# Kernel optimization log

Measured on AMD Instinct MI355X. Metric: run time of the kernel, lower is better.

The kernel has to match this reference:

```python
import jax, jax.numpy as jnp
import numpy as np

N = 50000      # num nodes
HID = 64       # hidden_dim
N2V = 64       # node2vec dim
E = 800000     # num edges
EP = 100000    # prediction edges
L = 2          # num_layers
EPS = 1e-5     # BatchNorm eps


def setup_inputs() -> dict:
    key = jax.random.key(0)
    ks = jax.random.split(key, 8)
    edge_index = jax.random.randint(ks[0], (2, E), 0, N)
    pred_edge = jax.random.randint(ks[1], (EP, 2), 0, N)
    id_emb = jax.random.normal(ks[2], (N, HID), jnp.float32) * 0.1      # learnable ID embedding
    n2v_emb = jax.random.normal(ks[3], (N, N2V), jnp.float32) * 0.1     # frozen node2vec embedding
    proj_w = jax.random.normal(ks[4], (HID + N2V, HID), jnp.float32) / np.sqrt(HID + N2V)
    proj_b = jnp.zeros((HID,), jnp.float32)
    conv_w = jax.random.normal(ks[5], (L, HID, HID), jnp.float32) / np.sqrt(HID)
    conv_b = jnp.zeros((L, HID), jnp.float32)
    bn_gamma = jnp.ones((L, HID), jnp.float32)
    bn_beta = jnp.zeros((L, HID), jnp.float32)
    return {"edge_index": edge_index, "pred_edge": pred_edge, "id_emb": id_emb,
            "n2v_emb": n2v_emb, "proj_w": proj_w, "proj_b": proj_b,
            "conv_w": conv_w, "conv_b": conv_b, "bn_gamma": bn_gamma, "bn_beta": bn_beta}


def reference(edge_index, pred_edge, id_emb, n2v_emb, proj_w, proj_b, conv_w, conv_b, bn_gamma, bn_beta):
    # input projection of concatenated embeddings: [N, HID+N2V] @ [HID+N2V, HID]
    x = jnp.concatenate([id_emb, n2v_emb], axis=1) @ proj_w + proj_b

    # GCN normalization with self-loops: norm_e = d^-1/2[src] * d^-1/2[dst]
    loops = jnp.arange(N, dtype=edge_index.dtype)
    row = jnp.concatenate([edge_index[0], loops])   # source nodes
    col = jnp.concatenate([edge_index[1], loops])   # destination nodes
    deg = jax.ops.segment_sum(jnp.ones(row.shape, x.dtype), col, num_segments=N)
    dis = jnp.where(deg > 0, jax.lax.rsqrt(deg), 0.0)
    norm = dis[row] * dis[col]                      # [E+N]

    for l in range(L):
        h = x @ conv_w[l]                                                    # [N, HID]
        agg = jax.ops.segment_sum(norm[:, None] * h[row], col, num_segments=N) + conv_b[l]
        # BatchNorm1d (training-mode batch stats over nodes)
        mu = agg.mean(axis=0)
        var = agg.var(axis=0)
        xn = (agg - mu) * jax.lax.rsqrt(var + EPS) * bn_gamma[l] + bn_beta[l]
        x = x + jax.nn.relu(xn)                                              # residual (shapes match)

    # dot-product link decoder
    z = x
    return (z[pred_edge[:, 0]] * z[pred_edge[:, 1]]).sum(axis=1)
```

## Files before the change

### kernel.cpp

```cpp
#include <hip/hip_runtime.h>

#define NN 50000
#define HID 64
#define NE 800000
#define NP 100000
#define BN_EPS 1e-5f
#define NB1 196

static inline size_t alignup(size_t x) { return (x + 255) & ~(size_t)255; }

__device__ __forceinline__ void f4fma(float a, const float4& w, float4& c) {
    c.x += a * w.x; c.y += a * w.y; c.z += a * w.z; c.w += a * w.w;
}
__device__ __forceinline__ void f4add(const float4& a, float4& c) {
    c.x += a.x; c.y += a.y; c.z += a.z; c.w += a.w;
}
__device__ __forceinline__ unsigned bfpack(float a, float b) {
    unsigned ua = __float_as_uint(a), ub = __float_as_uint(b);
    ua = (ua + 0x7fffu + ((ua >> 16) & 1u)) >> 16;
    ub = (ub + 0x7fffu + ((ub >> 16) & 1u)) >> 16;
    return ua | (ub << 16);
}
__device__ __forceinline__ float4 bf2f4(uint2 u) {
    float4 r;
    r.x = __uint_as_float(u.x << 16);
    r.y = __uint_as_float(u.x & 0xffff0000u);
    r.z = __uint_as_float(u.y << 16);
    r.w = __uint_as_float(u.y & 0xffff0000u);
    return r;
}


__global__ __launch_bounds__(256) void k_zero(int* __restrict__ cnt, float* __restrict__ sums,
                                              int* __restrict__ cursor) {
    int i = blockIdx.x * blockDim.x + threadIdx.x;
    if (i < NN) cnt[i] = 0;
    if (i < 256) sums[i] = 0.f;
    if (i == 0) *cursor = 0;
}


__global__ __launch_bounds__(256) void k_count(const int* __restrict__ col,
                                               int* __restrict__ cnt, int* __restrict__ rank) {
    int e = blockIdx.x * blockDim.x + threadIdx.x;
    if (e < NE) rank[e] = atomicAdd(&cnt[col[e]], 1);
}


__global__ __launch_bounds__(256) void k_alloc(const int* __restrict__ cnt,
                                               int* __restrict__ offs,
                                               float* __restrict__ dis,
                                               int* __restrict__ cursor) {
    __shared__ int s[256];
    __shared__ int base;
    int t = threadIdx.x;
    int i = blockIdx.x * 256 + t;
    int v = (i < NN) ? cnt[i] : 0;
    if (i < NN) dis[i] = rsqrtf((float)(v + 1));
    s[t] = v;
    __syncthreads();
    for (int off = 1; off < 256; off <<= 1) {
        int add = (t >= off) ? s[t - off] : 0;
        __syncthreads();
        s[t] += add;
        __syncthreads();
    }
    if (t == 255) base = atomicAdd(cursor, s[255]);
    __syncthreads();
    if (i < NN) offs[i] = base + s[t] - v;
}


__global__ __launch_bounds__(256) void k_fill(const int* __restrict__ row, const int* __restrict__ col,
                                              const int* __restrict__ rank, const int* __restrict__ offs,
                                              int* __restrict__ csr_src) {
    int e = blockIdx.x * blockDim.x + threadIdx.x;
    if (e >= NE) return;
    csr_src[offs[col[e]] + rank[e]] = row[e];
}


__global__ __launch_bounds__(256) void k_proj(const float* __restrict__ id_emb,
                                              const float* __restrict__ n2v,
                                              const float* __restrict__ W,
                                              const float* __restrict__ b,
                                              const float* __restrict__ dis,
                                              float* __restrict__ x,
                                              unsigned short* __restrict__ xh) {
    __shared__ float Wl[128 * 64];
    int tid = threadIdx.x;
    for (int i = tid; i < 128 * 64; i += 256) Wl[i] = W[i];
    __syncthreads();
    int sub = tid >> 4, q = tid & 15;
    const float4* W4 = (const float4*)Wl;
    const float4* id4 = (const float4*)id_emb;
    const float4* nv4 = (const float4*)n2v;
    float4* x4 = (float4*)x;
    uint2* xh2 = (uint2*)xh;
    float4 bb = ((const float4*)b)[q];
    const int ngroups = (NN + 63) / 64;
    for (int g = blockIdx.x; g < ngroups; g += gridDim.x) {
        int n0 = g * 64 + sub * 4;
        int r0 = min(n0 + 0, NN - 1), r1 = min(n0 + 1, NN - 1);
        int r2 = min(n0 + 2, NN - 1), r3 = min(n0 + 3, NN - 1);
        float4 c0 = bb, c1 = bb, c2 = bb, c3 = bb;
#pragma unroll 4
        for (int k4 = 0; k4 < 16; ++k4) {
            float4 a0 = id4[r0 * 16 + k4];
            float4 a1 = id4[r1 * 16 + k4];
            float4 a2 = id4[r2 * 16 + k4];
            float4 a3 = id4[r3 * 16 + k4];
            float4 w0 = W4[(k4 * 4 + 0) * 16 + q];
            float4 w1 = W4[(k4 * 4 + 1) * 16 + q];
            float4 w2 = W4[(k4 * 4 + 2) * 16 + q];
            float4 w3 = W4[(k4 * 4 + 3) * 16 + q];
            f4fma(a0.x, w0, c0); f4fma(a0.y, w1, c0); f4fma(a0.z, w2, c0); f4fma(a0.w, w3, c0);
            f4fma(a1.x, w0, c1); f4fma(a1.y, w1, c1); f4fma(a1.z, w2, c1); f4fma(a1.w, w3, c1);
            f4fma(a2.x, w0, c2); f4fma(a2.y, w1, c2); f4fma(a2.z, w2, c2); f4fma(a2.w, w3, c2);
            f4fma(a3.x, w0, c3); f4fma(a3.y, w1, c3); f4fma(a3.z, w2, c3); f4fma(a3.w, w3, c3);
        }
#pragma unroll 4
        for (int k4 = 0; k4 < 16; ++k4) {
            float4 a0 = nv4[r0 * 16 + k4];
            float4 a1 = nv4[r1 * 16 + k4];
            float4 a2 = nv4[r2 * 16 + k4];
            float4 a3 = nv4[r3 * 16 + k4];
            float4 w0 = W4[(k4 * 4 + 64) * 16 + q];
            float4 w1 = W4[(k4 * 4 + 65) * 16 + q];
            float4 w2 = W4[(k4 * 4 + 66) * 16 + q];
            float4 w3 = W4[(k4 * 4 + 67) * 16 + q];
            f4fma(a0.x, w0, c0); f4fma(a0.y, w1, c0); f4fma(a0.z, w2, c0); f4fma(a0.w, w3, c0);
            f4fma(a1.x, w0, c1); f4fma(a1.y, w1, c1); f4fma(a1.z, w2, c1); f4fma(a1.w, w3, c1);
            f4fma(a2.x, w0, c2); f4fma(a2.y, w1, c2); f4fma(a2.z, w2, c2); f4fma(a2.w, w3, c2);
            f4fma(a3.x, w0, c3); f4fma(a3.y, w1, c3); f4fma(a3.z, w2, c3); f4fma(a3.w, w3, c3);
        }
        if (n0 + 0 < NN) { float d = dis[n0+0]; x4[(n0+0)*16+q] = c0;
            xh2[(n0+0)*16+q] = make_uint2(bfpack(c0.x*d,c0.y*d), bfpack(c0.z*d,c0.w*d)); }
        if (n0 + 1 < NN) { float d = dis[n0+1]; x4[(n0+1)*16+q] = c1;
            xh2[(n0+1)*16+q] = make_uint2(bfpack(c1.x*d,c1.y*d), bfpack(c1.z*d,c1.w*d)); }
        if (n0 + 2 < NN) { float d = dis[n0+2]; x4[(n0+2)*16+q] = c2;
            xh2[(n0+2)*16+q] = make_uint2(bfpack(c2.x*d,c2.y*d), bfpack(c2.z*d,c2.w*d)); }
        if (n0 + 3 < NN) { float d = dis[n0+3]; x4[(n0+3)*16+q] = c3;
            xh2[(n0+3)*16+q] = make_uint2(bfpack(c3.x*d,c3.y*d), bfpack(c3.z*d,c3.w*d)); }
    }
}


__global__ __launch_bounds__(256) void k_gather(const int* __restrict__ offs,
                                                const int* __restrict__ cnt,
                                                const int* __restrict__ csr_src,
                                                const float* __restrict__ dis,
                                                const unsigned short* __restrict__ xh,
                                                unsigned short* __restrict__ th) {
    int gw = (blockIdx.x * blockDim.x + threadIdx.x) >> 6;
    int lane = threadIdx.x & 63;
    int sub = lane >> 4, q = lane & 15;
    int node = gw * 4 + sub;
    if (node >= NN) return;
    const uint2* xh2 = (const uint2*)xh;
    float4 acc = make_float4(0.f, 0.f, 0.f, 0.f);
    int j = offs[node], j1 = j + cnt[node];
    for (; j + 7 < j1; j += 8) {
        int s0 = csr_src[j],     s1 = csr_src[j + 1], s2 = csr_src[j + 2], s3 = csr_src[j + 3];
        int s4 = csr_src[j + 4], s5 = csr_src[j + 5], s6 = csr_src[j + 6], s7 = csr_src[j + 7];
        uint2 u0 = xh2[s0 * 16 + q];
        uint2 u1 = xh2[s1 * 16 + q];
        uint2 u2 = xh2[s2 * 16 + q];
        uint2 u3 = xh2[s3 * 16 + q];
        uint2 u4 = xh2[s4 * 16 + q];
        uint2 u5 = xh2[s5 * 16 + q];
        uint2 u6 = xh2[s6 * 16 + q];
        uint2 u7 = xh2[s7 * 16 + q];
        f4add(bf2f4(u0), acc); f4add(bf2f4(u1), acc);
        f4add(bf2f4(u2), acc); f4add(bf2f4(u3), acc);
        f4add(bf2f4(u4), acc); f4add(bf2f4(u5), acc);
        f4add(bf2f4(u6), acc); f4add(bf2f4(u7), acc);
    }
    for (; j < j1; ++j) {
        uint2 u0 = xh2[csr_src[j] * 16 + q];
        f4add(bf2f4(u0), acc);
    }
    f4add(bf2f4(xh2[node * 16 + q]), acc);
    float di = dis[node];
    acc.x *= di; acc.y *= di; acc.z *= di; acc.w *= di;
    ((uint2*)th)[node * 16 + q] = make_uint2(bfpack(acc.x, acc.y), bfpack(acc.z, acc.w));
}


__global__ __launch_bounds__(256) void k_gemm_stats(const unsigned short* __restrict__ th,
                                                    const float* __restrict__ W,
                                                    float* __restrict__ agg,
                                                    float* __restrict__ sums) {
    __shared__ float Wl[64 * 64];
    __shared__ float ls0[16][64];
    __shared__ float ls1[16][64];
    int tid = threadIdx.x;
    for (int i = tid; i < 64 * 64; i += 256) Wl[i] = W[i];
    __syncthreads();
    int sub = tid >> 4, q = tid & 15;
    const uint2* t2 = (const uint2*)th;
    const float4* W4 = (const float4*)Wl;
    float4* agg4 = (float4*)agg;
    float4 s1 = make_float4(0.f, 0.f, 0.f, 0.f), s2 = s1;
    const int ngroups = (NN + 63) / 64;
    for (int g = blockIdx.x; g < ngroups; g += gridDim.x) {
        int n0 = g * 64 + sub * 4;
        int r0 = min(n0 + 0, NN - 1), r1 = min(n0 + 1, NN - 1);
        int r2 = min(n0 + 2, NN - 1), r3 = min(n0 + 3, NN - 1);
        float4 c0 = make_float4(0.f,0.f,0.f,0.f), c1 = c0, c2 = c0, c3 = c0;
#pragma unroll 4
        for (int k4 = 0; k4 < 16; ++k4) {
            float4 a0 = bf2f4(t2[r0 * 16 + k4]);
            float4 a1 = bf2f4(t2[r1 * 16 + k4]);
            float4 a2 = bf2f4(t2[r2 * 16 + k4]);
            float4 a3 = bf2f4(t2[r3 * 16 + k4]);
            float4 w0 = W4[(k4 * 4 + 0) * 16 + q];
            float4 w1 = W4[(k4 * 4 + 1) * 16 + q];
            float4 w2 = W4[(k4 * 4 + 2) * 16 + q];
            float4 w3 = W4[(k4 * 4 + 3) * 16 + q];
            f4fma(a0.x, w0, c0); f4fma(a0.y, w1, c0); f4fma(a0.z, w2, c0); f4fma(a0.w, w3, c0);
            f4fma(a1.x, w0, c1); f4fma(a1.y, w1, c1); f4fma(a1.z, w2, c1); f4fma(a1.w, w3, c1);
            f4fma(a2.x, w0, c2); f4fma(a2.y, w1, c2); f4fma(a2.z, w2, c2); f4fma(a2.w, w3, c2);
            f4fma(a3.x, w0, c3); f4fma(a3.y, w1, c3); f4fma(a3.z, w2, c3); f4fma(a3.w, w3, c3);
        }
        if (n0 + 0 < NN) { agg4[(n0 + 0) * 16 + q] = c0;
            s1.x += c0.x; s1.y += c0.y; s1.z += c0.z; s1.w += c0.w;
            s2.x += c0.x*c0.x; s2.y += c0.y*c0.y; s2.z += c0.z*c0.z; s2.w += c0.w*c0.w; }
        if (n0 + 1 < NN) { agg4[(n0 + 1) * 16 + q] = c1;
            s1.x += c1.x; s1.y += c1.y; s1.z += c1.z; s1.w += c1.w;
            s2.x += c1.x*c1.x; s2.y += c1.y*c1.y; s2.z += c1.z*c1.z; s2.w += c1.w*c1.w; }
        if (n0 + 2 < NN) { agg4[(n0 + 2) * 16 + q] = c2;
            s1.x += c2.x; s1.y += c2.y; s1.z += c2.z; s1.w += c2.w;
            s2.x += c2.x*c2.x; s2.y += c2.y*c2.y; s2.z += c2.z*c2.z; s2.w += c2.w*c2.w; }
        if (n0 + 3 < NN) { agg4[(n0 + 3) * 16 + q] = c3;
            s1.x += c3.x; s1.y += c3.y; s1.z += c3.z; s1.w += c3.w;
            s2.x += c3.x*c3.x; s2.y += c3.y*c3.y; s2.z += c3.z*c3.z; s2.w += c3.w*c3.w; }
    }
    ls0[sub][q * 4 + 0] = s1.x; ls0[sub][q * 4 + 1] = s1.y;
    ls0[sub][q * 4 + 2] = s1.z; ls0[sub][q * 4 + 3] = s1.w;
    ls1[sub][q * 4 + 0] = s2.x; ls1[sub][q * 4 + 1] = s2.y;
    ls1[sub][q * 4 + 2] = s2.z; ls1[sub][q * 4 + 3] = s2.w;
    __syncthreads();
    if (tid < 64) {
        float a = 0.f;
#pragma unroll
        for (int r = 0; r < 16; ++r) a += ls0[r][tid];
        atomicAdd(&sums[tid], a);
    } else if (tid < 128) {
        int c = tid - 64;
        float a = 0.f;
#pragma unroll
        for (int r = 0; r < 16; ++r) a += ls1[r][c];
        atomicAdd(&sums[64 + c], a);
    }
}


__global__ __launch_bounds__(256) void k_bnupdate(const float* __restrict__ agg,
                                                  const float* __restrict__ sums,
                                                  const float* __restrict__ gamma,
                                                  const float* __restrict__ beta,
                                                  const float* __restrict__ dis,
                                                  int prescale,
                                                  float* __restrict__ x,
                                                  unsigned short* __restrict__ xh) {
    int i = blockIdx.x * blockDim.x + threadIdx.x;
    if (i >= NN * 16) return;
    int f4 = i & 15;
    const float invn = 1.0f / (float)NN;
    float4 sm = ((const float4*)sums)[f4];
    float4 sq = ((const float4*)(sums + 64))[f4];
    float4 g = ((const float4*)gamma)[f4];
    float4 be = ((const float4*)beta)[f4];
    float4 a = ((const float4*)agg)[i];
    float4 xv = ((const float4*)x)[i];
    float mu, var, rstd, xn;
    mu = sm.x * invn; var = sq.x * invn - mu * mu; rstd = rsqrtf(var + BN_EPS);
    xn = (a.x - mu) * rstd * g.x + be.x; xv.x += fmaxf(xn, 0.f);
    mu = sm.y * invn; var = sq.y * invn - mu * mu; rstd = rsqrtf(var + BN_EPS);
    xn = (a.y - mu) * rstd * g.y + be.y; xv.y += fmaxf(xn, 0.f);
    mu = sm.z * invn; var = sq.z * invn - mu * mu; rstd = rsqrtf(var + BN_EPS);
    xn = (a.z - mu) * rstd * g.z + be.z; xv.z += fmaxf(xn, 0.f);
    mu = sm.w * invn; var = sq.w * invn - mu * mu; rstd = rsqrtf(var + BN_EPS);
    xn = (a.w - mu) * rstd * g.w + be.w; xv.w += fmaxf(xn, 0.f);
    ((float4*)x)[i] = xv;
    float d = prescale ? dis[i >> 4] : 1.0f;
    ((uint2*)xh)[i] = make_uint2(bfpack(xv.x * d, xv.y * d), bfpack(xv.z * d, xv.w * d));
}


__global__ __launch_bounds__(256) void k_decode(const int* __restrict__ pred,
                                                const unsigned short* __restrict__ zh,
                                                float* __restrict__ out) {
    int gw = (blockIdx.x * blockDim.x + threadIdx.x) >> 6;
    int lane = threadIdx.x & 63;
    int sub = lane >> 4, q = lane & 15;
    int p = gw * 4 + sub;
    if (p >= NP) return;
    const uint2* z2 = (const uint2*)zh;
    int a = pred[2 * p], b = pred[2 * p + 1];
    float4 va = bf2f4(z2[a * 16 + q]);
    float4 vb = bf2f4(z2[b * 16 + q]);
    float v = va.x * vb.x + va.y * vb.y + va.z * vb.z + va.w * vb.w;
    v += __shfl_xor(v, 1);
    v += __shfl_xor(v, 2);
    v += __shfl_xor(v, 4);
    v += __shfl_xor(v, 8);
    if (q == 0) out[p] = v;
}

extern "C" void kernel_launch(void* const* d_in, const int* in_sizes, int n_in,
                              void* d_out, int out_size, void* d_ws, size_t ws_size,
                              hipStream_t stream) {
    const int* edge_index = (const int*)d_in[0];
    const int* pred       = (const int*)d_in[1];
    const float* id_emb   = (const float*)d_in[2];
    const float* n2v      = (const float*)d_in[3];
    const float* proj_w   = (const float*)d_in[4];
    const float* proj_b   = (const float*)d_in[5];
    const float* conv_w   = (const float*)d_in[6];
    const float* gamma    = (const float*)d_in[8];
    const float* beta     = (const float*)d_in[9];
    float* out = (float*)d_out;

    char* ws = (char*)d_ws;
    size_t off = 0;
    float* dis   = (float*)(ws + off); off += alignup(NN * 4);
    int* cnt     = (int*)(ws + off);   off += alignup(NN * 4);
    int* offs    = (int*)(ws + off);   off += alignup(NN * 4);
    int* rank    = (int*)(ws + off);   off += alignup((size_t)NE * 4);
    int* cursor  = (int*)(ws + off);   off += alignup(4);
    int* csr_src = (int*)(ws + off);   off += alignup((size_t)NE * 4);
    float* x     = (float*)(ws + off); off += alignup((size_t)NN * 64 * 4);
    float* agg   = (float*)(ws + off); off += alignup((size_t)NN * 64 * 4);
    unsigned short* xh = (unsigned short*)(ws + off); off += alignup((size_t)NN * 64 * 2);
    unsigned short* th = (unsigned short*)(ws + off); off += alignup((size_t)NN * 64 * 2);
    float* sums  = (float*)(ws + off);

    const int* row = edge_index;
    const int* col = edge_index + NE;

    k_zero<<<NB1, 256, 0, stream>>>(cnt, sums, cursor);
    k_count<<<(NE + 255) / 256, 256, 0, stream>>>(col, cnt, rank);
    k_alloc<<<NB1, 256, 0, stream>>>(cnt, offs, dis, cursor);
    k_fill<<<(NE + 255) / 256, 256, 0, stream>>>(row, col, rank, offs, csr_src);

    k_proj<<<512, 256, 0, stream>>>(id_emb, n2v, proj_w, proj_b, dis, x, xh);

    for (int l = 0; l < 2; ++l) {
        k_gather<<<((NN + 3) / 4 * 64 + 255) / 256, 256, 0, stream>>>(offs, cnt, csr_src, dis, xh, th);
        k_gemm_stats<<<512, 256, 0, stream>>>(th, conv_w + l * 64 * 64, agg, sums + l * 128);
        k_bnupdate<<<(NN * 16 + 255) / 256, 256, 0, stream>>>(agg, sums + l * 128, gamma + l * 64,
                                                              beta + l * 64, dis, (l == 0) ? 1 : 0, x, xh);
    }

    k_decode<<<(NP / 4 * 64 + 255) / 256, 256, 0, stream>>>(pred, xh, out);
}
```

Before: 205.0 us.

## Split bf16 feature tables into two 32-column planes and gather each separately

Stores the bf16 node feature and aggregate tables as two planes of 32 columns each, so each plane is half the size. The gather kernel runs twice, once per plane, with 8 lanes per node, which is meant to shrink the random-access working set so it fits better in cache. The projection weights are also held as bf16 in shared memory, and the projection launch becomes one block per 64-node group instead of a grid-stride loop. In exchange, the CSR index list is read twice per layer, there is an extra launch, and the projection weights lose precision.

```diff
diff --git a/kernel.cpp b/kernel.cpp
--- a/kernel.cpp
+++ b/kernel.cpp
@@ -6,6 +6,7 @@
 #define NP 100000
 #define BN_EPS 1e-5f
 #define NB1 196
+#define PLANE (NN * 32)
 
 static inline size_t alignup(size_t x) { return (x + 255) & ~(size_t)255; }
 
@@ -20,6 +21,10 @@
     ua = (ua + 0x7fffu + ((ua >> 16) & 1u)) >> 16;
     ub = (ub + 0x7fffu + ((ub >> 16) & 1u)) >> 16;
     return ua | (ub << 16);
+}
+__device__ __forceinline__ unsigned short bf1(float a) {
+    unsigned ua = __float_as_uint(a);
+    return (unsigned short)((ua + 0x7fffu + ((ua >> 16) & 1u)) >> 16);
 }
 __device__ __forceinline__ float4 bf2f4(uint2 u) {
     float4 r;
@@ -87,29 +92,132 @@
                                               const float* __restrict__ dis,
                                               float* __restrict__ x,
                                               unsigned short* __restrict__ xh) {
-    __shared__ float Wl[128 * 64];
+    __shared__ unsigned short Wlh[128 * 64];
     int tid = threadIdx.x;
-    for (int i = tid; i < 128 * 64; i += 256) Wl[i] = W[i];
+    for (int i = tid; i < 128 * 64; i += 256) Wlh[i] = bf1(W[i]);
     __syncthreads();
     int sub = tid >> 4, q = tid & 15;
-    const float4* W4 = (const float4*)Wl;
+    const uint2* W2 = (const uint2*)Wlh;
     const float4* id4 = (const float4*)id_emb;
     const float4* nv4 = (const float4*)n2v;
     float4* x4 = (float4*)x;
-    uint2* xh2 = (uint2*)xh;
+    uint2* xp = (uint2*)(xh + (q < 8 ? 0 : PLANE));
+    int qq = q & 7;
     float4 bb = ((const float4*)b)[q];
+    int n0 = blockIdx.x * 64 + sub * 4;
+    int r0 = min(n0 + 0, NN - 1), r1 = min(n0 + 1, NN - 1);
+    int r2 = min(n0 + 2, NN - 1), r3 = min(n0 + 3, NN - 1);
+    float4 c0 = bb, c1 = bb, c2 = bb, c3 = bb;
+#pragma unroll 4
+    for (int k4 = 0; k4 < 16; ++k4) {
+        float4 a0 = id4[r0 * 16 + k4];
+        float4 a1 = id4[r1 * 16 + k4];
+        float4 a2 = id4[r2 * 16 + k4];
+        float4 a3 = id4[r3 * 16 + k4];
+        float4 w0 = bf2f4(W2[(k4 * 4 + 0) * 16 + q]);
+        float4 w1 = bf2f4(W2[(k4 * 4 + 1) * 16 + q]);
+        float4 w2 = bf2f4(W2[(k4 * 4 + 2) * 16 + q]);
+        float4 w3 = bf2f4(W2[(k4 * 4 + 3) * 16 + q]);
+        f4fma(a0.x, w0, c0); f4fma(a0.y, w1, c0); f4fma(a0.z, w2, c0); f4fma(a0.w, w3, c0);
+        f4fma(a1.x, w0, c1); f4fma(a1.y, w1, c1); f4fma(a1.z, w2, c1); f4fma(a1.w, w3, c1);
+        f4fma(a2.x, w0, c2); f4fma(a2.y, w1, c2); f4fma(a2.z, w2, c2); f4fma(a2.w, w3, c2);
+        f4fma(a3.x, w0, c3); f4fma(a3.y, w1, c3); f4fma(a3.z, w2, c3); f4fma(a3.w, w3, c3);
+    }
+#pragma unroll 4
+    for (int k4 = 0; k4 < 16; ++k4) {
+        float4 a0 = nv4[r0 * 16 + k4];
+        float4 a1 = nv4[r1 * 16 + k4];
+        float4 a2 = nv4[r2 * 16 + k4];
+        float4 a3 = nv4[r3 * 16 + k4];
+        float4 w0 = bf2f4(W2[(k4 * 4 + 64) * 16 + q]);
+        float4 w1 = bf2f4(W2[(k4 * 4 + 65) * 16 + q]);
+        float4 w2 = bf2f4(W2[(k4 * 4 + 66) * 16 + q]);
+        float4 w3 = bf2f4(W2[(k4 * 4 + 67) * 16 + q]);
+        f4fma(a0.x, w0, c0); f4fma(a0.y, w1, c0); f4fma(a0.z, w2, c0); f4fma(a0.w, w3, c0);
+        f4fma(a1.x, w0, c1); f4fma(a1.y, w1, c1); f4fma(a1.z, w2, c1); f4fma(a1.w, w3, c1);
+        f4fma(a2.x, w0, c2); f4fma(a2.y, w1, c2); f4fma(a2.z, w2, c2); f4fma(a2.w, w3, c2);
+        f4fma(a3.x, w0, c3); f4fma(a3.y, w1, c3); f4fma(a3.z, w2, c3); f4fma(a3.w, w3, c3);
+    }
+    if (n0 + 0 < NN) { float d = dis[n0+0]; x4[(n0+0)*16+q] = c0;
+        xp[(n0+0)*8+qq] = make_uint2(bfpack(c0.x*d,c0.y*d), bfpack(c0.z*d,c0.w*d)); }
+    if (n0 + 1 < NN) { float d = dis[n0+1]; x4[(n0+1)*16+q] = c1;
+        xp[(n0+1)*8+qq] = make_uint2(bfpack(c1.x*d,c1.y*d), bfpack(c1.z*d,c1.w*d)); }
+    if (n0 + 2 < NN) { float d = dis[n0+2]; x4[(n0+2)*16+q] = c2;
+        xp[(n0+2)*8+qq] = make_uint2(bfpack(c2.x*d,c2.y*d), bfpack(c2.z*d,c2.w*d)); }
+    if (n0 + 3 < NN) { float d = dis[n0+3]; x4[(n0+3)*16+q] = c3;
+        xp[(n0+3)*8+qq] = make_uint2(bfpack(c3.x*d,c3.y*d), bfpack(c3.z*d,c3.w*d)); }
+}
+
+
+__global__ __launch_bounds__(256) void k_gather(const int* __restrict__ offs,
+                                                const int* __restrict__ cnt,
+                                                const int* __restrict__ csr_src,
+                                                const float* __restrict__ dis,
+                                                const unsigned short* __restrict__ xh_p,
+                                                unsigned short* __restrict__ th_p) {
+    int gw = (blockIdx.x * blockDim.x + threadIdx.x) >> 6;
+    int lane = threadIdx.x & 63;
+    int node = gw * 8 + (lane >> 3);
+    int q = lane & 7;
+    if (node >= NN) return;
+    const uint2* x2 = (const uint2*)xh_p;
+    float4 acc = make_float4(0.f, 0.f, 0.f, 0.f);
+    int j = offs[node], j1 = j + cnt[node];
+    for (; j + 7 < j1; j += 8) {
+        int s0 = csr_src[j],     s1 = csr_src[j + 1], s2 = csr_src[j + 2], s3 = csr_src[j + 3];
+        int s4 = csr_src[j + 4], s5 = csr_src[j + 5], s6 = csr_src[j + 6], s7 = csr_src[j + 7];
+        uint2 u0 = x2[s0 * 8 + q];
+        uint2 u1 = x2[s1 * 8 + q];
+        uint2 u2 = x2[s2 * 8 + q];
+        uint2 u3 = x2[s3 * 8 + q];
+        uint2 u4 = x2[s4 * 8 + q];
+        uint2 u5 = x2[s5 * 8 + q];
+        uint2 u6 = x2[s6 * 8 + q];
+        uint2 u7 = x2[s7 * 8 + q];
+        f4add(bf2f4(u0), acc); f4add(bf2f4(u1), acc);
+        f4add(bf2f4(u2), acc); f4add(bf2f4(u3), acc);
+        f4add(bf2f4(u4), acc); f4add(bf2f4(u5), acc);
+        f4add(bf2f4(u6), acc); f4add(bf2f4(u7), acc);
+    }
+    for (; j < j1; ++j) {
+        uint2 u0 = x2[csr_src[j] * 8 + q];
+        f4add(bf2f4(u0), acc);
+    }
+    f4add(bf2f4(x2[node * 8 + q]), acc);
+    float di = dis[node];
+    acc.x *= di; acc.y *= di; acc.z *= di; acc.w *= di;
+    ((uint2*)th_p)[node * 8 + q] = make_uint2(bfpack(acc.x, acc.y), bfpack(acc.z, acc.w));
+}
+
+
+__global__ __launch_bounds__(256) void k_gemm_stats(const unsigned short* __restrict__ th,
+                                                    const float* __restrict__ W,
+                                                    float* __restrict__ agg,
+                                                    float* __restrict__ sums) {
+    __shared__ float Wl[64 * 64];
+    __shared__ float ls0[16][64];
+    __shared__ float ls1[16][64];
+    int tid = threadIdx.x;
+    for (int i = tid; i < 64 * 64; i += 256) Wl[i] = W[i];
+    __syncthreads();
+    int sub = tid >> 4, q = tid & 15;
+    const uint2* t0 = (const uint2*)th;
+    const uint2* t1 = (const uint2*)(th + PLANE);
+    const float4* W4 = (const float4*)Wl;
+    float4* agg4 = (float4*)agg;
+    float4 s1 = make_float4(0.f, 0.f, 0.f, 0.f), s2 = s1;
     const int ngroups = (NN + 63) / 64;
     for (int g = blockIdx.x; g < ngroups; g += gridDim.x) {
         int n0 = g * 64 + sub * 4;
         int r0 = min(n0 + 0, NN - 1), r1 = min(n0 + 1, NN - 1);
         int r2 = min(n0 + 2, NN - 1), r3 = min(n0 + 3, NN - 1);
-        float4 c0 = bb, c1 = bb, c2 = bb, c3 = bb;
+        float4 c0 = make_float4(0.f,0.f,0.f,0.f), c1 = c0, c2 = c0, c3 = c0;
 #pragma unroll 4
-        for (int k4 = 0; k4 < 16; ++k4) {
-            float4 a0 = id4[r0 * 16 + k4];
-            float4 a1 = id4[r1 * 16 + k4];
-            float4 a2 = id4[r2 * 16 + k4];
-            float4 a3 = id4[r3 * 16 + k4];
+        for (int k4 = 0; k4 < 8; ++k4) {
+            float4 a0 = bf2f4(t0[r0 * 8 + k4]);
+            float4 a1 = bf2f4(t0[r1 * 8 + k4]);
+            float4 a2 = bf2f4(t0[r2 * 8 + k4]);
+            float4 a3 = bf2f4(t0[r3 * 8 + k4]);
             float4 w0 = W4[(k4 * 4 + 0) * 16 + q];
             float4 w1 = W4[(k4 * 4 + 1) * 16 + q];
             float4 w2 = W4[(k4 * 4 + 2) * 16 + q];
@@ -120,104 +228,15 @@
             f4fma(a3.x, w0, c3); f4fma(a3.y, w1, c3); f4fma(a3.z, w2, c3); f4fma(a3.w, w3, c3);
         }
 #pragma unroll 4
-        for (int k4 = 0; k4 < 16; ++k4) {
-            float4 a0 = nv4[r0 * 16 + k4];
-            float4 a1 = nv4[r1 * 16 + k4];
-            float4 a2 = nv4[r2 * 16 + k4];
-            float4 a3 = nv4[r3 * 16 + k4];
-            float4 w0 = W4[(k4 * 4 + 64) * 16 + q];
-            float4 w1 = W4[(k4 * 4 + 65) * 16 + q];
-            float4 w2 = W4[(k4 * 4 + 66) * 16 + q];
-            float4 w3 = W4[(k4 * 4 + 67) * 16 + q];
-            f4fma(a0.x, w0, c0); f4fma(a0.y, w1, c0); f4fma(a0.z, w2, c0); f4fma(a0.w, w3, c0);
-            f4fma(a1.x, w0, c1); f4fma(a1.y, w1, c1); f4fma(a1.z, w2, c1); f4fma(a1.w, w3, c1);
-            f4fma(a2.x, w0, c2); f4fma(a2.y, w1, c2); f4fma(a2.z, w2, c2); f4fma(a2.w, w3, c2);
-            f4fma(a3.x, w0, c3); f4fma(a3.y, w1, c3); f4fma(a3.z, w2, c3); f4fma(a3.w, w3, c3);
-        }
-        if (n0 + 0 < NN) { float d = dis[n0+0]; x4[(n0+0)*16+q] = c0;
-            xh2[(n0+0)*16+q] = make_uint2(bfpack(c0.x*d,c0.y*d), bfpack(c0.z*d,c0.w*d)); }
-        if (n0 + 1 < NN) { float d = dis[n0+1]; x4[(n0+1)*16+q] = c1;
-            xh2[(n0+1)*16+q] = make_uint2(bfpack(c1.x*d,c1.y*d), bfpack(c1.z*d,c1.w*d)); }
-        if (n0 + 2 < NN) { float d = dis[n0+2]; x4[(n0+2)*16+q] = c2;
-            xh2[(n0+2)*16+q] = make_uint2(bfpack(c2.x*d,c2.y*d), bfpack(c2.z*d,c2.w*d)); }
-        if (n0 + 3 < NN) { float d = dis[n0+3]; x4[(n0+3)*16+q] = c3;
-            xh2[(n0+3)*16+q] = make_uint2(bfpack(c3.x*d,c3.y*d), bfpack(c3.z*d,c3.w*d)); }
-    }
-}
-
-
-__global__ __launch_bounds__(256) void k_gather(const int* __restrict__ offs,
-                                                const int* __restrict__ cnt,
-                                                const int* __restrict__ csr_src,
-                                                const float* __restrict__ dis,
-                                                const unsigned short* __restrict__ xh,
-                                                unsigned short* __restrict__ th) {
-    int gw = (blockIdx.x * blockDim.x + threadIdx.x) >> 6;
-    int lane = threadIdx.x & 63;
-    int sub = lane >> 4, q = lane & 15;
-    int node = gw * 4 + sub;
-    if (node >= NN) return;
-    const uint2* xh2 = (const uint2*)xh;
-    float4 acc = make_float4(0.f, 0.f, 0.f, 0.f);
-    int j = offs[node], j1 = j + cnt[node];
-    for (; j + 7 < j1; j += 8) {
-        int s0 = csr_src[j],     s1 = csr_src[j + 1], s2 = csr_src[j + 2], s3 = csr_src[j + 3];
-        int s4 = csr_src[j + 4], s5 = csr_src[j + 5], s6 = csr_src[j + 6], s7 = csr_src[j + 7];
-        uint2 u0 = xh2[s0 * 16 + q];
-        uint2 u1 = xh2[s1 * 16 + q];
-        uint2 u2 = xh2[s2 * 16 + q];
-        uint2 u3 = xh2[s3 * 16 + q];
-        uint2 u4 = xh2[s4 * 16 + q];
-        uint2 u5 = xh2[s5 * 16 + q];
-        uint2 u6 = xh2[s6 * 16 + q];
-        uint2 u7 = xh2[s7 * 16 + q];
-        f4add(bf2f4(u0), acc); f4add(bf2f4(u1), acc);
-        f4add(bf2f4(u2), acc); f4add(bf2f4(u3), acc);
-        f4add(bf2f4(u4), acc); f4add(bf2f4(u5), acc);
-        f4add(bf2f4(u6), acc); f4add(bf2f4(u7), acc);
-    }
-    for (; j < j1; ++j) {
-        uint2 u0 = xh2[csr_src[j] * 16 + q];
-        f4add(bf2f4(u0), acc);
-    }
-    f4add(bf2f4(xh2[node * 16 + q]), acc);
-    float di = dis[node];
-    acc.x *= di; acc.y *= di; acc.z *= di; acc.w *= di;
-    ((uint2*)th)[node * 16 + q] = make_uint2(bfpack(acc.x, acc.y), bfpack(acc.z, acc.w));
-}
-
-
-__global__ __launch_bounds__(256) void k_gemm_stats(const unsigned short* __restrict__ th,
-                                                    const float* __restrict__ W,
-                                                    float* __restrict__ agg,
-                                                    float* __restrict__ sums) {
-    __shared__ float Wl[64 * 64];
-    __shared__ float ls0[16][64];
-    __shared__ float ls1[16][64];
-    int tid = threadIdx.x;
-    for (int i = tid; i < 64 * 64; i += 256) Wl[i] = W[i];
-    __syncthreads();
-    int sub = tid >> 4, q = tid & 15;
-    const uint2* t2 = (const uint2*)th;
-    const float4* W4 = (const float4*)Wl;
-    float4* agg4 = (float4*)agg;
-    float4 s1 = make_float4(0.f, 0.f, 0.f, 0.f), s2 = s1;
-    const int ngroups = (NN + 63) / 64;
-    for (int g = blockIdx.x; g < ngroups; g += gridDim.x) {
-        int n0 = g * 64 + sub * 4;
-        int r0 = min(n0 + 0, NN - 1), r1 = min(n0 + 1, NN - 1);
-        int r2 = min(n0 + 2, NN - 1), r3 = min(n0 + 3, NN - 1);
-        float4 c0 = make_float4(0.f,0.f,0.f,0.f), c1 = c0, c2 = c0, c3 = c0;
-#pragma unroll 4
-        for (int k4 = 0; k4 < 16; ++k4) {
-            float4 a0 = bf2f4(t2[r0 * 16 + k4]);
-            float4 a1 = bf2f4(t2[r1 * 16 + k4]);
-            float4 a2 = bf2f4(t2[r2 * 16 + k4]);
-            float4 a3 = bf2f4(t2[r3 * 16 + k4]);
-            float4 w0 = W4[(k4 * 4 + 0) * 16 + q];
-            float4 w1 = W4[(k4 * 4 + 1) * 16 + q];
-            float4 w2 = W4[(k4 * 4 + 2) * 16 + q];
-            float4 w3 = W4[(k4 * 4 + 3) * 16 + q];
+        for (int k4 = 0; k4 < 8; ++k4) {
+            float4 a0 = bf2f4(t1[r0 * 8 + k4]);
+            float4 a1 = bf2f4(t1[r1 * 8 + k4]);
+            float4 a2 = bf2f4(t1[r2 * 8 + k4]);
+            float4 a3 = bf2f4(t1[r3 * 8 + k4]);
+            float4 w0 = W4[((k4 + 8) * 4 + 0) * 16 + q];
+            float4 w1 = W4[((k4 + 8) * 4 + 1) * 16 + q];
+            float4 w2 = W4[((k4 + 8) * 4 + 2) * 16 + q];
+            float4 w3 = W4[((k4 + 8) * 4 + 3) * 16 + q];
             f4fma(a0.x, w0, c0); f4fma(a0.y, w1, c0); f4fma(a0.z, w2, c0); f4fma(a0.w, w3, c0);
             f4fma(a1.x, w0, c1); f4fma(a1.y, w1, c1); f4fma(a1.z, w2, c1); f4fma(a1.w, w3, c1);
             f4fma(a2.x, w0, c2); f4fma(a2.y, w1, c2); f4fma(a2.z, w2, c2); f4fma(a2.w, w3, c2);
@@ -267,6 +286,7 @@
     int i = blockIdx.x * blockDim.x + threadIdx.x;
     if (i >= NN * 16) return;
     int f4 = i & 15;
+    int node = i >> 4;
     const float invn = 1.0f / (float)NN;
     float4 sm = ((const float4*)sums)[f4];
     float4 sq = ((const float4*)(sums + 64))[f4];
@@ -284,8 +304,9 @@
     mu = sm.w * invn; var = sq.w * invn - mu * mu; rstd = rsqrtf(var + BN_EPS);
     xn = (a.w - mu) * rstd * g.w + be.w; xv.w += fmaxf(xn, 0.f);
     ((float4*)x)[i] = xv;
-    float d = prescale ? dis[i >> 4] : 1.0f;
-    ((uint2*)xh)[i] = make_uint2(bfpack(xv.x * d, xv.y * d), bfpack(xv.z * d, xv.w * d));
+    float d = prescale ? dis[node] : 1.0f;
+    uint2* xp = (uint2*)(xh + (f4 < 8 ? 0 : PLANE));
+    xp[node * 8 + (f4 & 7)] = make_uint2(bfpack(xv.x * d, xv.y * d), bfpack(xv.z * d, xv.w * d));
 }
 
 
@@ -297,10 +318,11 @@
     int sub = lane >> 4, q = lane & 15;
     int p = gw * 4 + sub;
     if (p >= NP) return;
-    const uint2* z2 = (const uint2*)zh;
+    const uint2* zp = (const uint2*)(zh + (q < 8 ? 0 : PLANE));
+    int qq = q & 7;
     int a = pred[2 * p], b = pred[2 * p + 1];
-    float4 va = bf2f4(z2[a * 16 + q]);
-    float4 vb = bf2f4(z2[b * 16 + q]);
+    float4 va = bf2f4(zp[a * 8 + qq]);
+    float4 vb = bf2f4(zp[b * 8 + qq]);
     float v = va.x * vb.x + va.y * vb.y + va.z * vb.z + va.w * vb.w;
     v += __shfl_xor(v, 1);
     v += __shfl_xor(v, 2);
@@ -333,8 +355,8 @@
     int* csr_src = (int*)(ws + off);   off += alignup((size_t)NE * 4);
     float* x     = (float*)(ws + off); off += alignup((size_t)NN * 64 * 4);
     float* agg   = (float*)(ws + off); off += alignup((size_t)NN * 64 * 4);
-    unsigned short* xh = (unsigned short*)(ws + off); off += alignup((size_t)NN * 64 * 2);
-    unsigned short* th = (unsigned short*)(ws + off); off += alignup((size_t)NN * 64 * 2);
+    unsigned short* xh = (unsigned short*)(ws + off); off += alignup((size_t)2 * PLANE * 2);
+    unsigned short* th = (unsigned short*)(ws + off); off += alignup((size_t)2 * PLANE * 2);
     float* sums  = (float*)(ws + off);
 
     const int* row = edge_index;
@@ -345,11 +367,13 @@
     k_alloc<<<NB1, 256, 0, stream>>>(cnt, offs, dis, cursor);
     k_fill<<<(NE + 255) / 256, 256, 0, stream>>>(row, col, rank, offs, csr_src);
 
-    k_proj<<<512, 256, 0, stream>>>(id_emb, n2v, proj_w, proj_b, dis, x, xh);
-
+    k_proj<<<(NN + 63) / 64, 256, 0, stream>>>(id_emb, n2v, proj_w, proj_b, dis, x, xh);
+
+    const int gather_blocks = ((NN + 7) / 8 * 64 + 255) / 256;
     for (int l = 0; l < 2; ++l) {
-        k_gather<<<((NN + 3) / 4 * 64 + 255) / 256, 256, 0, stream>>>(offs, cnt, csr_src, dis, xh, th);
-        k_gemm_stats<<<512, 256, 0, stream>>>(th, conv_w + l * 64 * 64, agg, sums + l * 128);
+        k_gather<<<gather_blocks, 256, 0, stream>>>(offs, cnt, csr_src, dis, xh, th);
+        k_gather<<<gather_blocks, 256, 0, stream>>>(offs, cnt, csr_src, dis, xh + PLANE, th + PLANE);
+        k_gemm_stats<<<782, 256, 0, stream>>>(th, conv_w + l * 64 * 64, agg, sums + l * 128);
         k_bnupdate<<<(NN * 16 + 255) / 256, 256, 0, stream>>>(agg, sums + l * 128, gamma + l * 64,
                                                               beta + l * 64, dis, (l == 0) ? 1 : 0, x, xh);
     }
```

Result: slower. 226.0 us (+10.3%).
